# Optimization experiments

Hardware: AMD Instinct MI355X
Metric: run time of the kernel (lower is better)

The kernel has to match this reference:

```python
import jax, jax.numpy as jnp
import numpy as np

B, S, E, H, DQ = 8, 1024, 128, 8, 128  # batch, seq, embedding_dim, head_num, qkv_dim
HD = H * DQ  # 1024


def setup_inputs() -> dict:
    key = jax.random.key(0)
    ks = jax.random.split(key, 8)
    q = jax.random.normal(ks[0], (B, S, E), dtype=jnp.float32)
    k = jax.random.normal(ks[1], (B, S, E), dtype=jnp.float32)
    v = jax.random.normal(ks[2], (B, S, E), dtype=jnp.float32)
    mask = jnp.zeros((B, S), dtype=jnp.float32)  # rank2 ninf mask (additive)
    scale = 0.02
    Wq = jax.random.normal(ks[3], (HD, E), dtype=jnp.float32) * scale  # torch Linear weight [out,in]
    Wk = jax.random.normal(ks[4], (HD, E), dtype=jnp.float32) * scale
    Wv = jax.random.normal(ks[5], (HD, E), dtype=jnp.float32) * scale
    Wc = jax.random.normal(ks[6], (E, HD), dtype=jnp.float32) * scale
    bc = jax.random.normal(ks[7], (E,), dtype=jnp.float32) * scale
    return {"q": q, "k": k, "v": v, "mask": mask,
            "Wq": Wq, "Wk": Wk, "Wv": Wv, "Wc": Wc, "bc": bc}


def reference(q, k, v, mask, Wq, Wk, Wv, Wc, bc):
    batch, n, emb = q.shape
    hd = Wq.shape[0]
    # Faithful to source quirk: head_num recomputed as out_features // in_features
    head_num = hd // emb
    BIG = 1e9
    EPS = 1e-12

    def heads(x):  # [B, n, HD] -> [B, H, n, d]
        return x.reshape(batch, -1, head_num, hd // head_num).transpose(0, 2, 1, 3)

    qh = heads(q @ Wq.T)
    kh = heads(k @ Wk.T)
    vh = heads(v @ Wv.T)
    d = qh.shape[-1]

    score = jnp.einsum('bhnd,bhmd->bhnm', qh, kh) / jnp.sqrt(jnp.float32(d))
    score = score + mask[:, None, None, :]
    score = jnp.nan_to_num(score, nan=-BIG, posinf=BIG, neginf=-BIG)
    w = jax.nn.softmax(score, axis=-1)
    w = jnp.nan_to_num(w, nan=0.0, posinf=0.0, neginf=0.0)
    w = jnp.maximum(w, 0.0)
    row_sum = jnp.sum(w, axis=-1, keepdims=True)
    # zero-row fallback: replace fully-masked rows with tiny uniform weights
    w = jnp.where(row_sum <= 0.0, EPS, w)
    row_sum = jnp.sum(w, axis=-1, keepdims=True)
    w = w / (row_sum + EPS)

    out = jnp.einsum('bhnm,bhmd->bhnd', w, vh)  # [B,H,n,d]
    out_concat = out.transpose(0, 2, 1, 3).reshape(batch, n, hd)
    return out_concat @ Wc.T + bc
```

## Files before the change

### kernel.cpp

```cpp
#include <hip/hip_runtime.h>

typedef __bf16 bf16;
typedef __attribute__((ext_vector_type(8))) __bf16 bf16x8;
typedef __attribute__((ext_vector_type(4))) __bf16 bf16x4;
typedef __attribute__((ext_vector_type(4))) float f32x4;

constexpr int Bb = 8;
constexpr int Ss = 1024;
constexpr int Ee = 128;
constexpr int Hh = 8;
constexpr int Dd = 128;
constexpr int HD = 1024;

__global__ void k_cvt(const float* __restrict__ q, const float* __restrict__ k,
                      const float* __restrict__ v, const float* __restrict__ Wq,
                      const float* __restrict__ Wk, const float* __restrict__ Wv,
                      bf16* __restrict__ xq, bf16* __restrict__ xk, bf16* __restrict__ xv,
                      bf16* __restrict__ Wqb, bf16* __restrict__ Wkb, bf16* __restrict__ Wvb)
{
    int gid = blockIdx.x * 256 + threadIdx.x;
    const float* src; bf16* dst; int off; float s = 1.0f;
    if      (gid < 262144) { src = q;  dst = xq;  off = gid; }
    else if (gid < 524288) { src = k;  dst = xk;  off = gid - 262144; }
    else if (gid < 786432) { src = v;  dst = xv;  off = gid - 524288; }
    else if (gid < 819200) { src = Wq; dst = Wqb; off = gid - 786432; s = 0.08838834764831845f; }
    else if (gid < 851968) { src = Wk; dst = Wkb; off = gid - 819200; }
    else                   { src = Wv; dst = Wvb; off = gid - 851968; }
    float4 f = ((const float4*)src)[off];
    bf16x4 p;
    p[0] = (bf16)(f.x * s); p[1] = (bf16)(f.y * s);
    p[2] = (bf16)(f.z * s); p[3] = (bf16)(f.w * s);
    ((bf16x4*)dst)[off] = p;
}

__global__ __launch_bounds__(256, 2) void k_qkv(
    const bf16* __restrict__ xq, const bf16* __restrict__ xk, const bf16* __restrict__ xv,
    const bf16* __restrict__ Wqb, const bf16* __restrict__ Wkb, const bf16* __restrict__ Wvb,
    bf16* __restrict__ Qh, bf16* __restrict__ Kh, bf16* __restrict__ Vt)
{
    const int rb    = blockIdx.x;
    const int h     = blockIdx.y;
    const int which = blockIdx.z;
    const bf16* x = (which == 0) ? xq  : (which == 1) ? xk  : xv;
    const bf16* W = (which == 0) ? Wqb : (which == 1) ? Wkb : Wvb;

    __shared__ bf16 Xs[128][136];
    __shared__ bf16 Ws[128][136];

    const int tid  = threadIdx.x;
    const int wv   = tid >> 6;
    const int lane = tid & 63;
    const int lo   = lane & 15;
    const int q4   = lane >> 4;

#pragma unroll
    for (int t = 0; t < 8; ++t) {
        int c = tid + t * 256;
        int row = c >> 4, c8 = (c & 15) << 3;
        *(bf16x8*)&Xs[row][c8] = *(const bf16x8*)&x[(rb * 128 + row) * Ee + c8];
        *(bf16x8*)&Ws[row][c8] = *(const bf16x8*)&W[(h * 128 + row) * Ee + c8];
    }
    __syncthreads();

    const bf16 (*Ap)[136] = (which == 2) ? Ws : Xs;
    const bf16 (*Bp)[136] = (which == 2) ? Xs : Ws;

    f32x4 acc[2][8];
#pragma unroll
    for (int i = 0; i < 2; ++i)
#pragma unroll
        for (int j = 0; j < 8; ++j) acc[i][j] = f32x4{0.f, 0.f, 0.f, 0.f};

#pragma unroll
    for (int kq = 0; kq < 4; ++kq) {
        bf16x8 a[2], b8[8];
#pragma unroll
        for (int ri = 0; ri < 2; ++ri)
            a[ri] = *(const bf16x8*)&Ap[wv * 32 + ri * 16 + lo][kq * 32 + q4 * 8];
#pragma unroll
        for (int cj = 0; cj < 8; ++cj)
            b8[cj] = *(const bf16x8*)&Bp[cj * 16 + lo][kq * 32 + q4 * 8];
#pragma unroll
        for (int ri = 0; ri < 2; ++ri)
#pragma unroll
            for (int cj = 0; cj < 8; ++cj)
                acc[ri][cj] = __builtin_amdgcn_mfma_f32_16x16x32_bf16(
                    a[ri], b8[cj], acc[ri][cj], 0, 0, 0);
    }

    const int bb = rb >> 3;
    const int s0 = (rb & 7) * 128;
    if (which < 2) {
        bf16* dst = ((which == 0) ? Qh : Kh) + (bb * Hh + h) * Ss * Dd;
#pragma unroll
        for (int ri = 0; ri < 2; ++ri)
#pragma unroll
            for (int cj = 0; cj < 8; ++cj)
#pragma unroll
                for (int r = 0; r < 4; ++r) {
                    int row = wv * 32 + ri * 16 + q4 * 4 + r;
                    int col = cj * 16 + lo;
                    dst[(s0 + row) * Dd + col] = (bf16)acc[ri][cj][r];
                }
    } else {
        bf16* dst = Vt + (bb * Hh + h) * Dd * Ss;
#pragma unroll
        for (int ri = 0; ri < 2; ++ri)
#pragma unroll
            for (int cj = 0; cj < 8; ++cj)
#pragma unroll
                for (int r = 0; r < 4; ++r) {
                    int row = wv * 32 + ri * 16 + q4 * 4 + r;
                    int col = cj * 16 + lo;
                    dst[row * Ss + s0 + col] = (bf16)acc[ri][cj][r];
                }
    }
}

__global__ __launch_bounds__(512, 4) void k_attn(
    const bf16* __restrict__ Qh, const bf16* __restrict__ Kh, const bf16* __restrict__ Vt,
    const float* __restrict__ mask, bf16* __restrict__ oc)
{
    const int bh = blockIdx.x;
    const int qt = blockIdx.y;
    const int b  = bh >> 3;
    const int h  = bh & 7;
    const int tid  = threadIdx.x;
    const int wv   = tid >> 6;
    const int lane = tid & 63;
    const int lo   = lane & 15;
    const int q4   = lane >> 4;

    __shared__ bf16 Ks[64][136];
    __shared__ bf16 Vs[128][72];
    __shared__ bf16 Ps[8][16][72];
    __shared__ float maskS[1024];

    const bf16* Qb = Qh + bh * Ss * Dd;
    const bf16* Kb = Kh + bh * Ss * Dd;
    const bf16* Vb = Vt + bh * Dd * Ss;

#pragma unroll
    for (int t = 0; t < 2; ++t)
        maskS[tid + t * 512] = mask[b * Ss + tid + t * 512];

    const int q0 = qt * 128 + wv * 16;
    bf16x8 qf[4];
#pragma unroll
    for (int kq = 0; kq < 4; ++kq)
        qf[kq] = *(const bf16x8*)&Qb[(q0 + lo) * Dd + kq * 32 + q4 * 8];

    f32x4 accO[8];
#pragma unroll
    for (int j = 0; j < 8; ++j) accO[j] = f32x4{0.f, 0.f, 0.f, 0.f};
    float lsum[4] = {0.f, 0.f, 0.f, 0.f};

    for (int kt = 0; kt < 16; ++kt) {
        const int j0 = kt * 64;
#pragma unroll
        for (int t = 0; t < 2; ++t) {
            int c = tid + t * 512;
            int row = c >> 4, c8 = (c & 15) << 3;
            *(bf16x8*)&Ks[row][c8] = *(const bf16x8*)&Kb[(j0 + row) * Dd + c8];
        }
#pragma unroll
        for (int t = 0; t < 2; ++t) {
            int c = tid + t * 512;
            int row = c >> 3, c8 = (c & 7) << 3;
            *(bf16x8*)&Vs[row][c8] = *(const bf16x8*)&Vb[row * Ss + j0 + c8];
        }
        __syncthreads();

        f32x4 sc[4];
#pragma unroll
        for (int j = 0; j < 4; ++j) sc[j] = f32x4{0.f, 0.f, 0.f, 0.f};
#pragma unroll
        for (int kq = 0; kq < 4; ++kq) {
            bf16x8 kf[4];
#pragma unroll
            for (int cj = 0; cj < 4; ++cj)
                kf[cj] = *(const bf16x8*)&Ks[cj * 16 + lo][kq * 32 + q4 * 8];
#pragma unroll
            for (int cj = 0; cj < 4; ++cj)
                sc[cj] = __builtin_amdgcn_mfma_f32_16x16x32_bf16(
                    qf[kq], kf[cj], sc[cj], 0, 0, 0);
        }

        float mv[4];
#pragma unroll
        for (int cj = 0; cj < 4; ++cj) mv[cj] = maskS[j0 + cj * 16 + lo];

#pragma unroll
        for (int r = 0; r < 4; ++r) {
            float p[4];
#pragma unroll
            for (int cj = 0; cj < 4; ++cj) p[cj] = __expf(sc[cj][r] + mv[cj]);
            lsum[r] += (p[0] + p[1]) + (p[2] + p[3]);
            const int prow = q4 * 4 + r;
#pragma unroll
            for (int cj = 0; cj < 4; ++cj)
                Ps[wv][prow][cj * 16 + lo] = (bf16)p[cj];
        }

#pragma unroll
        for (int kq = 0; kq < 2; ++kq) {
            bf16x8 pf = *(const bf16x8*)&Ps[wv][lo][kq * 32 + q4 * 8];
#pragma unroll
            for (int cj = 0; cj < 8; ++cj) {
                bf16x8 vf = *(const bf16x8*)&Vs[cj * 16 + lo][kq * 32 + q4 * 8];
                accO[cj] = __builtin_amdgcn_mfma_f32_16x16x32_bf16(
                    pf, vf, accO[cj], 0, 0, 0);
            }
        }
        __syncthreads();
    }

#pragma unroll
    for (int r = 0; r < 4; ++r) {
#pragma unroll
        for (int off = 1; off < 16; off <<= 1)
            lsum[r] += __shfl_xor(lsum[r], off, 64);
        float inv = 1.0f / (lsum[r] + 1e-12f);
        int sg = qt * 128 + wv * 16 + q4 * 4 + r;
        bf16* dst = oc + (b * Ss + sg) * HD + h * 128;
#pragma unroll
        for (int cj = 0; cj < 8; ++cj)
            dst[cj * 16 + lo] = (bf16)(accO[cj][r] * inv);
    }
}

__global__ __launch_bounds__(256, 4) void k_proj(
    const bf16* __restrict__ oc, const float* __restrict__ Wc,
    const float* __restrict__ bc, float* __restrict__ out)
{
    const int mt   = blockIdx.x;
    const int tid  = threadIdx.x;
    const int wv   = tid >> 6;
    const int lane = tid & 63;
    const int lo   = lane & 15;
    const int q4   = lane >> 4;

    f32x4 acc[2];
    acc[0] = f32x4{0.f, 0.f, 0.f, 0.f};
    acc[1] = f32x4{0.f, 0.f, 0.f, 0.f};

    const bf16* arow = oc + (mt * 16 + lo) * HD + q4 * 8;

    for (int kc = 0; kc < 8; ++kc) {
        const int k0 = kc * 128;
        bf16x8 a[4];
#pragma unroll
        for (int kq = 0; kq < 4; ++kq)
            a[kq] = *(const bf16x8*)&arow[k0 + kq * 32];
#pragma unroll
        for (int cj = 0; cj < 2; ++cj) {
            const int n = wv * 32 + cj * 16 + lo;
#pragma unroll
            for (int kq = 0; kq < 4; ++kq) {
                const float* wp = &Wc[n * HD + k0 + kq * 32 + q4 * 8];
                float4 f0 = *(const float4*)wp;
                float4 f1 = *(const float4*)(wp + 4);
                bf16x8 bfr;
                bfr[0] = (bf16)f0.x; bfr[1] = (bf16)f0.y; bfr[2] = (bf16)f0.z; bfr[3] = (bf16)f0.w;
                bfr[4] = (bf16)f1.x; bfr[5] = (bf16)f1.y; bfr[6] = (bf16)f1.z; bfr[7] = (bf16)f1.w;
                acc[cj] = __builtin_amdgcn_mfma_f32_16x16x32_bf16(
                    a[kq], bfr, acc[cj], 0, 0, 0);
            }
        }
    }

#pragma unroll
    for (int cj = 0; cj < 2; ++cj) {
        int col = wv * 32 + cj * 16 + lo;
        float bias = bc[col];
#pragma unroll
        for (int r = 0; r < 4; ++r) {
            int row = mt * 16 + q4 * 4 + r;
            out[row * Ee + col] = acc[cj][r] + bias;
        }
    }
}

extern "C" void kernel_launch(void* const* d_in, const int* in_sizes, int n_in,
                              void* d_out, int out_size, void* d_ws, size_t ws_size,
                              hipStream_t stream)
{
    const float* q    = (const float*)d_in[0];
    const float* k    = (const float*)d_in[1];
    const float* v    = (const float*)d_in[2];
    const float* mask = (const float*)d_in[3];
    const float* Wq   = (const float*)d_in[4];
    const float* Wk   = (const float*)d_in[5];
    const float* Wv   = (const float*)d_in[6];
    const float* Wc   = (const float*)d_in[7];
    const float* bc   = (const float*)d_in[8];
    float* out = (float*)d_out;

    constexpr int NBH = Bb * Hh * Ss * Dd;
    bf16* Qh = (bf16*)d_ws;
    bf16* Kh = Qh + NBH;
    bf16* Vt = Kh + NBH;
    bf16* oc = Vt + NBH;
    bf16* xq  = oc;
    bf16* xk  = xq + Bb * Ss * Ee;
    bf16* xv  = xk + Bb * Ss * Ee;
    bf16* Wqb = xv + Bb * Ss * Ee;
    bf16* Wkb = Wqb + HD * Ee;
    bf16* Wvb = Wkb + HD * Ee;

    k_cvt<<<dim3(3456), 256, 0, stream>>>(q, k, v, Wq, Wk, Wv, xq, xk, xv, Wqb, Wkb, Wvb);
    k_qkv<<<dim3(64, 8, 3), 256, 0, stream>>>(xq, xk, xv, Wqb, Wkb, Wvb, Qh, Kh, Vt);
    k_attn<<<dim3(64, 8), 512, 0, stream>>>(Qh, Kh, Vt, mask, oc);
    k_proj<<<dim3(512), 256, 0, stream>>>(oc, Wc, bc, out);
}
```

Measured before the change: 186.9 us.

## Fuse input conversion into QKV GEMM and restructure attention with direct-to-LDS loads

```diff
diff --git a/kernel.cpp b/kernel.cpp
--- a/kernel.cpp
+++ b/kernel.cpp
@@ -12,20 +12,21 @@
 constexpr int Dd = 128;
 constexpr int HD = 1024;
 
-__global__ void k_cvt(const float* __restrict__ q, const float* __restrict__ k,
-                      const float* __restrict__ v, const float* __restrict__ Wq,
-                      const float* __restrict__ Wk, const float* __restrict__ Wv,
-                      bf16* __restrict__ xq, bf16* __restrict__ xk, bf16* __restrict__ xv,
+__device__ __forceinline__ void gl_lds16(const bf16* gp, bf16* lp) {
+    __builtin_amdgcn_global_load_lds(
+        (const __attribute__((address_space(1))) unsigned int*)gp,
+        (__attribute__((address_space(3))) unsigned int*)lp, 16, 0, 0);
+}
+
+__global__ void k_cvt(const float* __restrict__ Wq, const float* __restrict__ Wk,
+                      const float* __restrict__ Wv,
                       bf16* __restrict__ Wqb, bf16* __restrict__ Wkb, bf16* __restrict__ Wvb)
 {
     int gid = blockIdx.x * 256 + threadIdx.x;
     const float* src; bf16* dst; int off; float s = 1.0f;
-    if      (gid < 262144) { src = q;  dst = xq;  off = gid; }
-    else if (gid < 524288) { src = k;  dst = xk;  off = gid - 262144; }
-    else if (gid < 786432) { src = v;  dst = xv;  off = gid - 524288; }
-    else if (gid < 819200) { src = Wq; dst = Wqb; off = gid - 786432; s = 0.08838834764831845f; }
-    else if (gid < 851968) { src = Wk; dst = Wkb; off = gid - 819200; }
-    else                   { src = Wv; dst = Wvb; off = gid - 851968; }
+    if      (gid < 32768) { src = Wq; dst = Wqb; off = gid;         s = 0.12751741530603157f; }
+    else if (gid < 65536) { src = Wk; dst = Wkb; off = gid - 32768; }
+    else                  { src = Wv; dst = Wvb; off = gid - 65536; }
     float4 f = ((const float4*)src)[off];
     bf16x4 p;
     p[0] = (bf16)(f.x * s); p[1] = (bf16)(f.y * s);
@@ -34,15 +35,15 @@
 }
 
 __global__ __launch_bounds__(256, 2) void k_qkv(
-    const bf16* __restrict__ xq, const bf16* __restrict__ xk, const bf16* __restrict__ xv,
+    const float* __restrict__ qin, const float* __restrict__ kin, const float* __restrict__ vin,
     const bf16* __restrict__ Wqb, const bf16* __restrict__ Wkb, const bf16* __restrict__ Wvb,
     bf16* __restrict__ Qh, bf16* __restrict__ Kh, bf16* __restrict__ Vt)
 {
     const int rb    = blockIdx.x;
     const int h     = blockIdx.y;
     const int which = blockIdx.z;
-    const bf16* x = (which == 0) ? xq  : (which == 1) ? xk  : xv;
-    const bf16* W = (which == 0) ? Wqb : (which == 1) ? Wkb : Wvb;
+    const float* x = (which == 0) ? qin : (which == 1) ? kin : vin;
+    const bf16*  W = (which == 0) ? Wqb : (which == 1) ? Wkb : Wvb;
 
     __shared__ bf16 Xs[128][136];
     __shared__ bf16 Ws[128][136];
@@ -57,7 +58,13 @@
     for (int t = 0; t < 8; ++t) {
         int c = tid + t * 256;
         int row = c >> 4, c8 = (c & 15) << 3;
-        *(bf16x8*)&Xs[row][c8] = *(const bf16x8*)&x[(rb * 128 + row) * Ee + c8];
+        const float* xp = &x[(rb * 128 + row) * Ee + c8];
+        float4 f0 = *(const float4*)xp;
+        float4 f1 = *(const float4*)(xp + 4);
+        bf16x8 p;
+        p[0] = (bf16)f0.x; p[1] = (bf16)f0.y; p[2] = (bf16)f0.z; p[3] = (bf16)f0.w;
+        p[4] = (bf16)f1.x; p[5] = (bf16)f1.y; p[6] = (bf16)f1.z; p[7] = (bf16)f1.w;
+        *(bf16x8*)&Xs[row][c8] = p;
         *(bf16x8*)&Ws[row][c8] = *(const bf16x8*)&W[(h * 128 + row) * Ee + c8];
     }
     __syncthreads();
@@ -117,7 +124,7 @@
     }
 }
 
-__global__ __launch_bounds__(512, 4) void k_attn(
+__global__ __launch_bounds__(256, 2) void k_attn(
     const bf16* __restrict__ Qh, const bf16* __restrict__ Kh, const bf16* __restrict__ Vt,
     const float* __restrict__ mask, bf16* __restrict__ oc)
 {
@@ -131,9 +138,9 @@
     const int lo   = lane & 15;
     const int q4   = lane >> 4;
 
-    __shared__ bf16 Ks[64][136];
-    __shared__ bf16 Vs[128][72];
-    __shared__ bf16 Ps[8][16][72];
+    __shared__ bf16 KsL[64 * 128];
+    __shared__ bf16 VsL[128 * 64];
+    __shared__ bf16 Ps[4][32][72];
     __shared__ float maskS[1024];
 
     const bf16* Qb = Qh + bh * Ss * Dd;
@@ -141,49 +148,65 @@
     const bf16* Vb = Vt + bh * Dd * Ss;
 
 #pragma unroll
-    for (int t = 0; t < 2; ++t)
-        maskS[tid + t * 512] = mask[b * Ss + tid + t * 512];
-
-    const int q0 = qt * 128 + wv * 16;
-    bf16x8 qf[4];
-#pragma unroll
-    for (int kq = 0; kq < 4; ++kq)
-        qf[kq] = *(const bf16x8*)&Qb[(q0 + lo) * Dd + kq * 32 + q4 * 8];
-
-    f32x4 accO[8];
-#pragma unroll
-    for (int j = 0; j < 8; ++j) accO[j] = f32x4{0.f, 0.f, 0.f, 0.f};
-    float lsum[4] = {0.f, 0.f, 0.f, 0.f};
+    for (int t = 0; t < 4; ++t)
+        maskS[tid + t * 256] = mask[b * Ss + tid + t * 256] * 1.4426950408889634f;
+
+    const int q0 = qt * 128 + wv * 32;
+    bf16x8 qf[2][4];
+#pragma unroll
+    for (int ri = 0; ri < 2; ++ri)
+#pragma unroll
+        for (int kq = 0; kq < 4; ++kq)
+            qf[ri][kq] = *(const bf16x8*)&Qb[(q0 + ri * 16 + lo) * Dd + kq * 32 + q4 * 8];
+
+    f32x4 accO[2][8];
+#pragma unroll
+    for (int i = 0; i < 2; ++i)
+#pragma unroll
+        for (int j = 0; j < 8; ++j) accO[i][j] = f32x4{0.f, 0.f, 0.f, 0.f};
+    float lsum[2][4];
+#pragma unroll
+    for (int i = 0; i < 2; ++i)
+#pragma unroll
+        for (int r = 0; r < 4; ++r) lsum[i][r] = 0.f;
+
+    const int sw = lo & 7;
 
     for (int kt = 0; kt < 16; ++kt) {
         const int j0 = kt * 64;
 #pragma unroll
-        for (int t = 0; t < 2; ++t) {
-            int c = tid + t * 512;
-            int row = c >> 4, c8 = (c & 15) << 3;
-            *(bf16x8*)&Ks[row][c8] = *(const bf16x8*)&Kb[(j0 + row) * Dd + c8];
-        }
-#pragma unroll
-        for (int t = 0; t < 2; ++t) {
-            int c = tid + t * 512;
-            int row = c >> 3, c8 = (c & 7) << 3;
-            *(bf16x8*)&Vs[row][c8] = *(const bf16x8*)&Vb[row * Ss + j0 + c8];
+        for (int t = 0; t < 4; ++t) {
+            int i = wv * 4 + t;
+            int row = i * 4 + (lane >> 4);
+            int g = (lane & 15) ^ (row & 7);
+            gl_lds16(Kb + (j0 + row) * Dd + g * 8, &KsL[i * 512]);
+        }
+#pragma unroll
+        for (int t = 0; t < 4; ++t) {
+            int i = wv * 4 + t;
+            int row = i * 8 + (lane >> 3);
+            int g = (lane & 7) ^ (row & 7);
+            gl_lds16(Vb + row * Ss + j0 + g * 8, &VsL[i * 512]);
         }
         __syncthreads();
 
-        f32x4 sc[4];
-#pragma unroll
-        for (int j = 0; j < 4; ++j) sc[j] = f32x4{0.f, 0.f, 0.f, 0.f};
+        f32x4 sc[2][4];
+#pragma unroll
+        for (int i = 0; i < 2; ++i)
+#pragma unroll
+            for (int j = 0; j < 4; ++j) sc[i][j] = f32x4{0.f, 0.f, 0.f, 0.f};
 #pragma unroll
         for (int kq = 0; kq < 4; ++kq) {
             bf16x8 kf[4];
 #pragma unroll
             for (int cj = 0; cj < 4; ++cj)
-                kf[cj] = *(const bf16x8*)&Ks[cj * 16 + lo][kq * 32 + q4 * 8];
-#pragma unroll
-            for (int cj = 0; cj < 4; ++cj)
-                sc[cj] = __builtin_amdgcn_mfma_f32_16x16x32_bf16(
-                    qf[kq], kf[cj], sc[cj], 0, 0, 0);
+                kf[cj] = *(const bf16x8*)&KsL[(cj * 16 + lo) * 128 + (((kq << 2) + q4) ^ sw) * 8];
+#pragma unroll
+            for (int ri = 0; ri < 2; ++ri)
+#pragma unroll
+                for (int cj = 0; cj < 4; ++cj)
+                    sc[ri][cj] = __builtin_amdgcn_mfma_f32_16x16x32_bf16(
+                        qf[ri][kq], kf[cj], sc[ri][cj], 0, 0, 0);
         }
 
         float mv[4];
@@ -191,42 +214,53 @@
         for (int cj = 0; cj < 4; ++cj) mv[cj] = maskS[j0 + cj * 16 + lo];
 
 #pragma unroll
+        for (int ri = 0; ri < 2; ++ri) {
+#pragma unroll
+            for (int r = 0; r < 4; ++r) {
+                float p[4];
+#pragma unroll
+                for (int cj = 0; cj < 4; ++cj) p[cj] = exp2f(sc[ri][cj][r] + mv[cj]);
+                lsum[ri][r] += (p[0] + p[1]) + (p[2] + p[3]);
+                const int prow = ri * 16 + q4 * 4 + r;
+#pragma unroll
+                for (int cj = 0; cj < 4; ++cj)
+                    Ps[wv][prow][cj * 16 + lo] = (bf16)p[cj];
+            }
+        }
+
+#pragma unroll
+        for (int kq = 0; kq < 2; ++kq) {
+            bf16x8 pf[2];
+#pragma unroll
+            for (int ri = 0; ri < 2; ++ri)
+                pf[ri] = *(const bf16x8*)&Ps[wv][ri * 16 + lo][kq * 32 + q4 * 8];
+#pragma unroll
+            for (int cj = 0; cj < 8; ++cj) {
+                bf16x8 vf = *(const bf16x8*)&VsL[(cj * 16 + lo) * 64 + (((kq << 2) + q4) ^ sw) * 8];
+#pragma unroll
+                for (int ri = 0; ri < 2; ++ri)
+                    accO[ri][cj] = __builtin_amdgcn_mfma_f32_16x16x32_bf16(
+                        pf[ri], vf, accO[ri][cj], 0, 0, 0);
+            }
+        }
+        __syncthreads();
+    }
+
+#pragma unroll
+    for (int ri = 0; ri < 2; ++ri)
+#pragma unroll
         for (int r = 0; r < 4; ++r) {
-            float p[4];
-#pragma unroll
-            for (int cj = 0; cj < 4; ++cj) p[cj] = __expf(sc[cj][r] + mv[cj]);
-            lsum[r] += (p[0] + p[1]) + (p[2] + p[3]);
-            const int prow = q4 * 4 + r;
-#pragma unroll
-            for (int cj = 0; cj < 4; ++cj)
-                Ps[wv][prow][cj * 16 + lo] = (bf16)p[cj];
-        }
-
-#pragma unroll
-        for (int kq = 0; kq < 2; ++kq) {
-            bf16x8 pf = *(const bf16x8*)&Ps[wv][lo][kq * 32 + q4 * 8];
-#pragma unroll
-            for (int cj = 0; cj < 8; ++cj) {
-                bf16x8 vf = *(const bf16x8*)&Vs[cj * 16 + lo][kq * 32 + q4 * 8];
-                accO[cj] = __builtin_amdgcn_mfma_f32_16x16x32_bf16(
-                    pf, vf, accO[cj], 0, 0, 0);
-            }
-        }
-        __syncthreads();
-    }
-
-#pragma unroll
-    for (int r = 0; r < 4; ++r) {
-#pragma unroll
-        for (int off = 1; off < 16; off <<= 1)
-            lsum[r] += __shfl_xor(lsum[r], off, 64);
-        float inv = 1.0f / (lsum[r] + 1e-12f);
-        int sg = qt * 128 + wv * 16 + q4 * 4 + r;
-        bf16* dst = oc + (b * Ss + sg) * HD + h * 128;
-#pragma unroll
-        for (int cj = 0; cj < 8; ++cj)
-            dst[cj * 16 + lo] = (bf16)(accO[cj][r] * inv);
-    }
+            float s = lsum[ri][r];
+#pragma unroll
+            for (int off = 1; off < 16; off <<= 1)
+                s += __shfl_xor(s, off, 64);
+            float inv = 1.0f / (s + 1e-12f);
+            int sg = q0 + ri * 16 + q4 * 4 + r;
+            bf16* dst = oc + (b * Ss + sg) * HD + h * 128;
+#pragma unroll
+            for (int cj = 0; cj < 8; ++cj)
+                dst[cj * 16 + lo] = (bf16)(accO[ri][cj][r] * inv);
+        }
 }
 
 __global__ __launch_bounds__(256, 4) void k_proj(
@@ -301,15 +335,12 @@
     bf16* Kh = Qh + NBH;
     bf16* Vt = Kh + NBH;
     bf16* oc = Vt + NBH;
-    bf16* xq  = oc;
-    bf16* xk  = xq + Bb * Ss * Ee;
-    bf16* xv  = xk + Bb * Ss * Ee;
-    bf16* Wqb = xv + Bb * Ss * Ee;
+    bf16* Wqb = oc;
     bf16* Wkb = Wqb + HD * Ee;
     bf16* Wvb = Wkb + HD * Ee;
 
-    k_cvt<<<dim3(3456), 256, 0, stream>>>(q, k, v, Wq, Wk, Wv, xq, xk, xv, Wqb, Wkb, Wvb);
-    k_qkv<<<dim3(64, 8, 3), 256, 0, stream>>>(xq, xk, xv, Wqb, Wkb, Wvb, Qh, Kh, Vt);
-    k_attn<<<dim3(64, 8), 512, 0, stream>>>(Qh, Kh, Vt, mask, oc);
+    k_cvt<<<dim3(384), 256, 0, stream>>>(Wq, Wk, Wv, Wqb, Wkb, Wvb);
+    k_qkv<<<dim3(64, 8, 3), 256, 0, stream>>>(q, k, v, Wqb, Wkb, Wvb, Qh, Kh, Vt);
+    k_attn<<<dim3(64, 8), 256, 0, stream>>>(Qh, Kh, Vt, mask, oc);
     k_proj<<<dim3(512), 256, 0, stream>>>(oc, Wc, bc, out);
 }
```

Result: faster. 180.8 us (-3.3%).
